# Kernel tuning notes

Hardware: AMD Instinct MI355X
Metric: run time of the kernel (lower is better)

## Reference

```python
import jax, jax.numpy as jnp
import numpy as np
from jax import lax

ANCHOR_SCALES = (64.0, 128.0, 256.0)
ANCHOR_RATIOS = (0.5, 1.0, 2.0)
STRIDE = 32
NMS_THRESH = 0.7


def make_anchors(feat_h, feat_w):
    base = []
    for s in ANCHOR_SCALES:
        for r in ANCHOR_RATIOS:
            w = s * np.sqrt(max(r, 1e-6))
            h = s / np.sqrt(max(r, 1e-6))
            base.append([-w / 2, -h / 2, w / 2, h / 2])
    base = jnp.asarray(base, jnp.float32)  # [A=9, 4]
    sx = jnp.arange(feat_w, dtype=jnp.float32) * STRIDE
    sy = jnp.arange(feat_h, dtype=jnp.float32) * STRIDE
    yy, xx = jnp.meshgrid(sy, sx, indexing='ij')
    shifts = jnp.stack([xx, yy, xx, yy], axis=2).reshape(-1, 4)  # [H*W, 4]
    # location-major, anchor-minor -> matches permute(0,2,3,1).view(B,-1,·)
    return (base[None, :, :] + shifts[:, None, :]).reshape(-1, 4)  # [N, 4]


def apply_deltas(anchors, deltas):
    w = anchors[:, 2] - anchors[:, 0]
    h = anchors[:, 3] - anchors[:, 1]
    cx = anchors[:, 0] + 0.5 * w
    cy = anchors[:, 1] + 0.5 * h
    pcx = deltas[:, 0] * w + cx
    pcy = deltas[:, 1] * h + cy
    pw = jnp.exp(deltas[:, 2]) * w
    ph = jnp.exp(deltas[:, 3]) * h
    return jnp.stack([pcx - 0.5 * pw, pcy - 0.5 * ph,
                      pcx + 0.5 * pw, pcy + 0.5 * ph], axis=1)


def pairwise_iou(b):
    area = (b[:, 2] - b[:, 0]) * (b[:, 3] - b[:, 1])
    lt = jnp.maximum(b[:, None, :2], b[None, :, :2])
    rb = jnp.minimum(b[:, None, 2:], b[None, :, 2:])
    wh = jnp.clip(rb - lt, 0.0)
    inter = wh[..., 0] * wh[..., 1]
    return inter / (area[:, None] + area[None, :] - inter)


def nms_keep(boxes, scores, thresh):
    # greedy NMS (torchvision semantics: suppress iou > thresh), returns bool keep mask
    n = boxes.shape[0]
    order = jnp.argsort(-scores)
    sb = boxes[order]
    idx = jnp.arange(n)
    sup_mat = (pairwise_iou(sb) > thresh) & (idx[None, :] > idx[:, None])

    def body(i, sup):
        return sup | ((~sup[i]) & sup_mat[i])

    sup = lax.fori_loop(0, n, body, jnp.zeros(n, bool))
    return jnp.zeros(n, bool).at[order].set(~sup)


def setup_inputs() -> dict:
    key = jax.random.key(0)
    ks = jax.random.split(key, 4)
    features = jax.random.normal(ks[0], (4, 512, 25, 25), jnp.float32)
    conv_w = jax.random.normal(ks[1], (512, 512, 3, 3), jnp.float32) * 0.01
    conv_b = jnp.zeros((512,), jnp.float32)
    cls_w = jax.random.normal(ks[2], (18, 512), jnp.float32) * 0.01
    cls_b = jnp.zeros((18,), jnp.float32)
    bbox_w = jax.random.normal(ks[3], (36, 512), jnp.float32) * 0.01
    bbox_b = jnp.zeros((36,), jnp.float32)
    return {"features": features, "conv_w": conv_w, "conv_b": conv_b,
            "cls_w": cls_w, "cls_b": cls_b, "bbox_w": bbox_w, "bbox_b": bbox_b,
            "img_h": 800, "img_w": 800}


def reference(features, conv_w, conv_b, cls_w, cls_b, bbox_w, bbox_b, img_h, img_w):
    B, _, H, W = features.shape
    x = lax.conv_general_dilated(features, conv_w, (1, 1), 'SAME',
                                 dimension_numbers=('NCHW', 'OIHW', 'NCHW'))
    x = jax.nn.relu(x + conv_b[None, :, None, None])
    obj = jnp.einsum('bchw,oc->bohw', x, cls_w) + cls_b[None, :, None, None]
    dlt = jnp.einsum('bchw,oc->bohw', x, bbox_w) + bbox_b[None, :, None, None]
    obj = obj.transpose(0, 2, 3, 1).reshape(B, -1, 2)      # [B, N, 2]
    dlt = dlt.transpose(0, 2, 3, 1).reshape(B, -1, 4)      # [B, N, 4]

    anchors = make_anchors(H, W)                            # [N, 4]
    props = jax.vmap(lambda d: apply_deltas(anchors, d))(dlt)
    hi = jnp.asarray([img_w, img_h, img_w, img_h], jnp.float32)
    props = jnp.clip(props, 0.0, hi)                        # clip to image
    scores = jax.nn.softmax(obj, axis=-1)[..., 1]           # [B, N]
    keep = jax.vmap(lambda b, s: nms_keep(b, s, NMS_THRESH))(props, scores)
    # suppressed boxes zeroed (fixed-shape analogue of props[keep])
    return props * keep[..., None].astype(props.dtype)
```

## Files before the change

### kernel.cpp

```cpp
#include <hip/hip_runtime.h>


#define NBATCH 4
#define HWDIM  25
#define NPOS   625
#define NM     2500
#define CIN    512
#define NANCH  5625
#define NW     88
#define CAP    4096
#define SORTN  6144

typedef unsigned long long u64;
typedef unsigned int u32;

struct BaseAnchors { float x1[9], y1[9], x2[9], y2[9]; };

__device__ __forceinline__ u64 bcast64(u64 v, int lane) {
  unsigned int lo = (unsigned int)v;
  unsigned int hi = (unsigned int)(v >> 32);
  lo = (unsigned int)__builtin_amdgcn_readlane((int)lo, lane);
  hi = (unsigned int)__builtin_amdgcn_readlane((int)hi, lane);
  return (((u64)hi) << 32) | (u64)lo;
}

__device__ __forceinline__ u64 waveOr64(u64 x) {
  unsigned int lo = (unsigned int)x, hi = (unsigned int)(x >> 32);
#pragma unroll
  for (int off = 32; off > 0; off >>= 1) {
    lo |= (unsigned int)__shfl_xor((int)lo, off, 64);
    hi |= (unsigned int)__shfl_xor((int)hi, off, 64);
  }
  return (((u64)hi) << 32) | (u64)lo;
}


__global__ void transpose_features(const float* __restrict__ f, float* __restrict__ fm) {
  __shared__ float tile[32][33];
  int b  = blockIdx.z;
  int p0 = blockIdx.x * 32;
  int c0 = blockIdx.y * 32;
  int tx = threadIdx.x, ty = threadIdx.y;
#pragma unroll
  for (int j = 0; j < 4; j++) {
    int c = c0 + ty + j * 8;
    int p = p0 + tx;
    if (p < NPOS) tile[ty + j * 8][tx] = f[((size_t)(b * CIN + c)) * NPOS + p];
  }
  __syncthreads();
#pragma unroll
  for (int j = 0; j < 4; j++) {
    int p = p0 + ty + j * 8;
    int c = c0 + tx;
    if (p < NPOS) fm[((size_t)(b * NPOS + p)) * CIN + c] = tile[tx][ty + j * 8];
  }
}

__global__ __launch_bounds__(256) void transpose_weights(const float* __restrict__ cw,
                                                         float* __restrict__ Wt) {
  __shared__ float tile[32][289];
  int o0 = blockIdx.x * 32, c0 = blockIdx.y * 32;
  int tid = threadIdx.x;
#pragma unroll
  for (int j = 0; j < 36; j++) {
    int idx = tid + j * 256;
    int o = idx / 288, kk = idx % 288;
    tile[o][kk] = cw[((size_t)(o0 + o)) * 4608 + c0 * 9 + kk];
  }
  __syncthreads();
  int ol = tid & 31, pg = tid >> 5;
#pragma unroll
  for (int j = 0; j < 36; j++) {
    int pair = pg + j * 8;
    int c = pair / 9, tap = pair % 9;
    Wt[((size_t)tap * CIN + (c0 + c)) * 512 + o0 + ol] = tile[ol][pair];
  }
}

__global__ void build_wco(const float* __restrict__ clsw, const float* __restrict__ clsb,
                          const float* __restrict__ bw, const float* __restrict__ bbb,
                          float* __restrict__ Wco, float* __restrict__ bco) {
  int idx = blockIdx.x * 256 + threadIdx.x;
  if (idx < 512 * 64) {
    int c = idx >> 6, o = idx & 63;
    float v = 0.f;
    if (o < 18) v = clsw[o * 512 + c];
    else if (o < 54) v = bw[(o - 18) * 512 + c];
    Wco[idx] = v;
  }
  if (idx < 64) {
    float v = 0.f;
    if (idx < 18) v = clsb[idx];
    else if (idx < 54) v = bbb[idx - 18];
    bco[idx] = v;
  }
}

__global__ void zero_cnt(u32* __restrict__ cnt) {
  int i = blockIdx.x * 64 + threadIdx.x;
  if (i < NBATCH * NW) cnt[i] = 0u;
}

__global__ __launch_bounds__(256) void conv_gemm(const float* __restrict__ fm,
                                                 const float* __restrict__ Wt,
                                                 float* __restrict__ xp) {
  __shared__ __align__(16) float At[32][68];
  __shared__ __align__(16) float Bt[32][64];
  int tid = threadIdx.x;
  int m0 = blockIdx.x << 6;
  int o0 = blockIdx.y << 6;
  int part = blockIdx.z;
  int ti = tid >> 4, tj = tid & 15;
  int si = tid >> 2, sq = tid & 3;
  int skk = tid >> 3, sr = tid & 7;
  float acc[4][4] = {{0.f}};

  int m = m0 + si;
  bool mv = m < NM;
  int mm = mv ? m : 0;
  int bb = mm / NPOS, rem = mm % NPOS;
  int hh = rem / HWDIM, ww = rem % HWDIM;
  int dy = part - 1;

  for (int tt = 0; tt < 3; tt++) {
    int tap = part * 3 + tt;
    int dx = tt - 1;
    int h2 = hh + dy, w2 = ww + dx;
    bool av = mv && ((unsigned)h2 < (unsigned)HWDIM) && ((unsigned)w2 < (unsigned)HWDIM);
    const float* arow = fm + (((size_t)(bb * NPOS + h2 * HWDIM + w2)) << 9);
    const float* bbase = Wt + (((size_t)tap) << 18) + o0;

    float4 a0 = make_float4(0.f, 0.f, 0.f, 0.f), a1 = a0;
    if (av) {
      a0 = *(const float4*)(arow + (sq << 2));
      a1 = *(const float4*)(arow + 16 + (sq << 2));
    }
    const float* bp0 = bbase + (((size_t)skk) << 9);
    float4 b0 = *(const float4*)(bp0 + (sr << 2));
    float4 b1 = *(const float4*)(bp0 + 32 + (sr << 2));

    for (int c0 = 0; c0 < CIN; c0 += 32) {
      __syncthreads();
      int kb = sq << 2;
      At[kb + 0][si] = a0.x; At[kb + 1][si] = a0.y; At[kb + 2][si] = a0.z; At[kb + 3][si] = a0.w;
      At[kb + 16][si] = a1.x; At[kb + 17][si] = a1.y; At[kb + 18][si] = a1.z; At[kb + 19][si] = a1.w;
      *(float4*)&Bt[skk][sr << 2] = b0;
      *(float4*)&Bt[skk][32 + (sr << 2)] = b1;
      float4 na0 = make_float4(0.f, 0.f, 0.f, 0.f), na1 = na0;
      float4 nb0 = na0, nb1 = na0;
      int c1 = c0 + 32;
      if (c1 < CIN) {
        if (av) {
          na0 = *(const float4*)(arow + c1 + (sq << 2));
          na1 = *(const float4*)(arow + c1 + 16 + (sq << 2));
        }
        const float* bp = bbase + (((size_t)(c1 + skk)) << 9);
        nb0 = *(const float4*)(bp + (sr << 2));
        nb1 = *(const float4*)(bp + 32 + (sr << 2));
      }
      __syncthreads();
#pragma unroll
      for (int kk = 0; kk < 32; kk++) {
        float4 avv = *(const float4*)&At[kk][ti << 2];
        float4 bvv = *(const float4*)&Bt[kk][tj << 2];
        float a_[4] = {avv.x, avv.y, avv.z, avv.w};
        float b_[4] = {bvv.x, bvv.y, bvv.z, bvv.w};
#pragma unroll
        for (int u = 0; u < 4; u++)
#pragma unroll
          for (int v = 0; v < 4; v++) acc[u][v] += a_[u] * b_[v];
      }
      a0 = na0; a1 = na1; b0 = nb0; b1 = nb1;
    }
  }
  float* outp = xp + (size_t)part * (NM * 512);
#pragma unroll
  for (int u = 0; u < 4; u++) {
    int mr = m0 + (ti << 2) + u;
    if (mr < NM) {
      float4 r = make_float4(acc[u][0], acc[u][1], acc[u][2], acc[u][3]);
      *(float4*)(outp + (((size_t)mr) << 9) + o0 + (tj << 2)) = r;
    }
  }
}

__global__ void combine_relu(const float* __restrict__ xp, const float* __restrict__ bias,
                             float* __restrict__ x2) {
  int i4 = blockIdx.x * 256 + threadIdx.x;
  if (i4 >= NM * 128) return;
  float4 p0 = *(const float4*)(xp + (size_t)i4 * 4);
  float4 p1 = *(const float4*)(xp + (size_t)(NM * 512) + (size_t)i4 * 4);
  float4 p2 = *(const float4*)(xp + (size_t)(2 * NM * 512) + (size_t)i4 * 4);
  float4 bb = *(const float4*)(bias + (i4 & 127) * 4);
  float4 r;
  r.x = fmaxf(p0.x + p1.x + p2.x + bb.x, 0.f);
  r.y = fmaxf(p0.y + p1.y + p2.y + bb.y, 0.f);
  r.z = fmaxf(p0.z + p1.z + p2.z + bb.z, 0.f);
  r.w = fmaxf(p0.w + p1.w + p2.w + bb.w, 0.f);
  *(float4*)(x2 + (size_t)i4 * 4) = r;
}

__global__ __launch_bounds__(256) void gemm1x1(const float* __restrict__ x2,
                                               const float* __restrict__ Wco,
                                               const float* __restrict__ bco,
                                               float* __restrict__ logits) {
  __shared__ __align__(16) float At[32][68];
  __shared__ __align__(16) float Bt[32][64];
  int tid = threadIdx.x;
  int m0 = blockIdx.x << 6;
  int ti = tid >> 4, tj = tid & 15;
  int si = tid >> 2, sq = tid & 3;
  int skk = tid >> 3, sr = tid & 7;
  float acc[4][4] = {{0.f}};
  int m = m0 + si;
  bool mv = m < NM;
  const float* arow = x2 + (((size_t)(mv ? m : 0)) << 9);
  for (int c0 = 0; c0 < CIN; c0 += 32) {
    __syncthreads();
    float4 a0 = make_float4(0.f, 0.f, 0.f, 0.f), a1 = a0;
    if (mv) {
      a0 = *(const float4*)(arow + c0 + (sq << 2));
      a1 = *(const float4*)(arow + c0 + 16 + (sq << 2));
    }
    int kb = sq << 2;
    At[kb + 0][si] = a0.x; At[kb + 1][si] = a0.y; At[kb + 2][si] = a0.z; At[kb + 3][si] = a0.w;
    At[kb + 16][si] = a1.x; At[kb + 17][si] = a1.y; At[kb + 18][si] = a1.z; At[kb + 19][si] = a1.w;
    const float* bp = Wco + (size_t)(c0 + skk) * 64;
    *(float4*)&Bt[skk][sr << 2] = *(const float4*)(bp + (sr << 2));
    *(float4*)&Bt[skk][32 + (sr << 2)] = *(const float4*)(bp + 32 + (sr << 2));
    __syncthreads();
#pragma unroll
    for (int kk = 0; kk < 32; kk++) {
      float4 avv = *(const float4*)&At[kk][ti << 2];
      float4 bvv = *(const float4*)&Bt[kk][tj << 2];
      float a_[4] = {avv.x, avv.y, avv.z, avv.w};
      float b_[4] = {bvv.x, bvv.y, bvv.z, bvv.w};
#pragma unroll
      for (int u = 0; u < 4; u++)
#pragma unroll
        for (int v = 0; v < 4; v++) acc[u][v] += a_[u] * b_[v];
    }
  }
  float4 bias = *(const float4*)(bco + (tj << 2));
#pragma unroll
  for (int u = 0; u < 4; u++) {
    int mr = m0 + (ti << 2) + u;
    if (mr < NM) {
      float4 r = make_float4(acc[u][0] + bias.x, acc[u][1] + bias.y, acc[u][2] + bias.z,
                             acc[u][3] + bias.w);
      *(float4*)(logits + (size_t)mr * 64 + (tj << 2)) = r;
    }
  }
}

__global__ __launch_bounds__(256) void score_box_kernel(const float* __restrict__ logits,
                                                        const int* __restrict__ ih,
                                                        const int* __restrict__ iw,
                                                        BaseAnchors ba,
                                                        float* __restrict__ scores,
                                                        float* __restrict__ props) {
#pragma clang fp contract(off)
  int n = blockIdx.x * 256 + threadIdx.x;
  if (n >= NBATCH * NANCH) return;
  int b = n / NANCH;
  int r = n % NANCH;
  int pos = r / 9, aa = r % 9;
  int py = pos / HWDIM, px = pos % HWDIM;
  const float* L = logits + (size_t)(b * NPOS + pos) * 64;
  float l0 = L[2 * aa], l1 = L[2 * aa + 1];
  float mx = fmaxf(l0, l1);
  float e0 = expf(l0 - mx), e1 = expf(l1 - mx);
  float s = e1 / (e0 + e1);
  float d0 = L[18 + 4 * aa + 0], d1 = L[18 + 4 * aa + 1];
  float d2 = L[18 + 4 * aa + 2], d3 = L[18 + 4 * aa + 3];
  float xf = (float)px * 32.f, yf = (float)py * 32.f;
  float ax1 = ba.x1[aa] + xf, ay1 = ba.y1[aa] + yf;
  float ax2 = ba.x2[aa] + xf, ay2 = ba.y2[aa] + yf;
  float wA = ax2 - ax1, hA = ay2 - ay1;
  float cx = ax1 + 0.5f * wA, cy = ay1 + 0.5f * hA;
  float pcx = d0 * wA + cx, pcy = d1 * hA + cy;
  float pw = expf(d2) * wA, ph = expf(d3) * hA;
  float x1 = pcx - 0.5f * pw, y1 = pcy - 0.5f * ph;
  float x2 = pcx + 0.5f * pw, y2 = pcy + 0.5f * ph;
  float W = (float)iw[0], H = (float)ih[0];
  x1 = fminf(fmaxf(x1, 0.f), W);
  y1 = fminf(fmaxf(y1, 0.f), H);
  x2 = fminf(fmaxf(x2, 0.f), W);
  y2 = fminf(fmaxf(y2, 0.f), H);
  scores[n] = s;
  *(float4*)(props + (size_t)n * 4) = make_float4(x1, y1, x2, y2);
}

__global__ __launch_bounds__(1024, 1) void radix_sort_kernel(const float* __restrict__ scores,
                                                             const float* __restrict__ props,
                                                             int* __restrict__ order,
                                                             float* __restrict__ sb) {
  __shared__ u32 kA[SORTN], vA[SORTN], kB[SORTN], vB[SORTN];
  __shared__ u32 hist[16][256];
  __shared__ u32 tot[256], base[256], tmp[256];
  int b = blockIdx.x, tid = threadIdx.x;
  int lane = tid & 63, wv = tid >> 6;
  const float* sc = scores + (size_t)b * NANCH;

  for (int i = tid; i < SORTN; i += 1024) {
    kA[i] = (i < NANCH) ? __float_as_uint(sc[i]) : 0u;
    vA[i] = (u32)i;
  }
  __syncthreads();

  for (int pass = 0; pass < 4; pass++) {
    int shift = pass << 3;
    u32* ks = (pass & 1) ? kB : kA;
    u32* vs = (pass & 1) ? vB : vA;
    u32* kd = (pass & 1) ? kA : kB;
    u32* vd = (pass & 1) ? vA : vB;
    for (int i = tid; i < 4096; i += 1024) ((u32*)hist)[i] = 0u;
    __syncthreads();
    for (int r = 0; r < 6; r++) {
      int i = wv * 384 + (r << 6) + lane;
      u32 d = 255u - ((ks[i] >> shift) & 255u);
      atomicAdd(&hist[wv][d], 1u);
    }
    __syncthreads();
    if (tid < 256) {
      u32 run = 0;
#pragma unroll
      for (int w = 0; w < 16; w++) { u32 t = hist[w][tid]; hist[w][tid] = run; run += t; }
      tot[tid] = run;
    }
    __syncthreads();
    if (tid < 256) tmp[tid] = tot[tid];
    __syncthreads();
    for (int off = 1; off < 256; off <<= 1) {
      u32 v = 0;
      if (tid < 256 && tid >= off) v = tmp[tid - off];
      __syncthreads();
      if (tid < 256) tmp[tid] += v;
      __syncthreads();
    }
    if (tid < 256) base[tid] = tmp[tid] - tot[tid];
    __syncthreads();
    if (tid < 256) {
      u32 bs = base[tid];
#pragma unroll
      for (int w = 0; w < 16; w++) hist[w][tid] += bs;
    }
    __syncthreads();
    for (int r = 0; r < 6; r++) {
      int i = wv * 384 + (r << 6) + lane;
      u32 key = ks[i], val = vs[i];
      u32 d = 255u - ((key >> shift) & 255u);
      u64 grp = ~0ull;
#pragma unroll
      for (int bit = 0; bit < 8; bit++) {
        u64 bal = __ballot(((d >> bit) & 1u) != 0u);
        grp &= ((d >> bit) & 1u) ? bal : ~bal;
      }
      u64 ltmask = (1ull << lane) - 1ull;
      u32 rank = (u32)__popcll(grp & ltmask);
      int leader = (int)__builtin_ctzll(grp);
      u32 oldv = 0;
      if (lane == leader) oldv = atomicAdd(&hist[wv][d], (u32)__popcll(grp));
      oldv = (u32)__shfl((int)oldv, leader, 64);
      u32 slot = oldv + rank;
      kd[slot] = key;
      vd[slot] = val;
    }
    __syncthreads();
  }

  const float* pr = props + (size_t)b * NANCH * 4;
  for (int i = tid; i < NANCH; i += 1024) {
    u32 orig = vA[i];
    order[b * NANCH + i] = (int)orig;
    float4 p = *(const float4*)(pr + (size_t)orig * 4);
    *(float4*)(sb + ((size_t)b * NANCH + i) * 4) = p;
  }
}

__global__ __launch_bounds__(64) void nms_mask_kernel(const float* __restrict__ sb,
                                                      uint4* __restrict__ lists,
                                                      u32* __restrict__ cnt,
                                                      u64* __restrict__ maskd) {
#pragma clang fp contract(off)
  int rb = blockIdx.x, cb = blockIdx.y, b = blockIdx.z;
  if (cb < rb) return;
  int lane = threadIdx.x;
  __shared__ float4 cbox[64];
  int j0 = cb << 6;
  const float* sbb = sb + (size_t)b * NANCH * 4;
  if (j0 + lane < NANCH) cbox[lane] = *(const float4*)(sbb + (size_t)(j0 + lane) * 4);
  __syncthreads();
  int i = (rb << 6) + lane;
  if (i >= NANCH) return;
  float4 rbox = *(const float4*)(sbb + (size_t)i * 4);
  float rarea = (rbox.z - rbox.x) * (rbox.w - rbox.y);
  u64 bits = 0ull;
  int jmax = NANCH - j0;
  if (jmax > 64) jmax = 64;
  for (int l = 0; l < jmax; l++) {
    int j = j0 + l;
    if (j > i) {
      float4 c = cbox[l];
      float carea = (c.z - c.x) * (c.w - c.y);
      float ltx = fmaxf(rbox.x, c.x), lty = fmaxf(rbox.y, c.y);
      float rbx = fminf(rbox.z, c.z), rby = fminf(rbox.w, c.w);
      float wx = fmaxf(rbx - ltx, 0.f);
      float wy = fmaxf(rby - lty, 0.f);
      float inter = wx * wy;
      float iou = inter / (rarea + carea - inter);
      if (iou > 0.7f) bits |= (1ull << l);
    }
  }
  if (rb == cb) {
    maskd[((size_t)b * NW + rb) * 64 + lane] = bits;
  } else if (bits) {
    u32 idx = atomicAdd(&cnt[b * NW + cb], 1u);
    if (idx < CAP)
      lists[((size_t)(b * NW + cb)) * CAP + idx] =
          make_uint4((u32)bits, (u32)(bits >> 32), (u32)i, 0u);
  }
}

__global__ __launch_bounds__(64, 1) void nms_scan_kernel(const uint4* __restrict__ lists,
                                                         const u32* __restrict__ cnt,
                                                         const u64* __restrict__ maskd,
                                                         const int* __restrict__ order,
                                                         const float* __restrict__ sb,
                                                         float* __restrict__ out) {
  int b = blockIdx.x;
  int lane = threadIdx.x;
  __shared__ u64 keep_sh[NW];
  const u64* md = maskd + (size_t)b * NW * 64;
  const uint4* lb = lists + (size_t)b * NW * CAP;

  u32 c0 = (lane < NW) ? cnt[b * NW + lane] : 0u;
  u32 c1 = (lane + 64 < NW) ? cnt[b * NW + lane + 64] : 0u;

  u64 diag = md[lane];
  uint4 pf = lb[lane];
  for (int s = 0; s < NW; s++) {
    u64 Mw = diag;
    uint4 e0 = pf;
    if (s + 1 < NW) {
      diag = md[((s + 1) << 6) + lane];
      pf = lb[(size_t)(s + 1) * CAP + lane];
    }

    int cn = (int)(u32)__builtin_amdgcn_readlane(
        (int)((s < 64) ? c0 : c1), (s < 64) ? s : s - 64);
    if (cn > CAP) cn = CAP;

    u64 acc = 0ull;
    if (lane < cn) {
      u64 kw = keep_sh[e0.z >> 6];
      if ((kw >> (e0.z & 63)) & 1ull) acc |= (((u64)e0.y) << 32) | (u64)e0.x;
    }
    for (int p = lane + 64; p < cn; p += 64) {
      uint4 e = lb[(size_t)s * CAP + p];
      u64 kw = keep_sh[e.z >> 6];
      if ((kw >> (e.z & 63)) & 1ull) acc |= (((u64)e.y) << 32) | (u64)e.x;
    }
    u64 cur = waveOr64(acc);

    int nrows = NANCH - (s << 6);
    if (nrows > 64) nrows = 64;
    u64 valid = (nrows < 64) ? ((1ull << nrows) - 1ull) : ~0ull;

    u64 nz = __ballot(Mw != 0ull);
    u64 todo = nz & ~cur & valid;
    while (todo) {
      int t = (int)__builtin_ctzll(todo);
      cur |= bcast64(Mw, t);
      todo &= ~cur;
      todo &= ~(1ull << t);
    }
    u64 alive = (~cur) & valid;
    if (lane == 0) keep_sh[s] = alive;
  }

  for (int i = lane; i < NANCH; i += 64) {
    u64 kw = keep_sh[i >> 6];
    bool kept = ((kw >> (i & 63)) & 1ull) != 0ull;
    int orig = order[b * NANCH + i];
    float4 p = *(const float4*)(sb + ((size_t)b * NANCH + i) * 4);
    float4 o = kept ? p : make_float4(0.f, 0.f, 0.f, 0.f);
    *(float4*)(out + ((size_t)b * NANCH + orig) * 4) = o;
  }
}


extern "C" void kernel_launch(void* const* d_in, const int* in_sizes, int n_in,
                              void* d_out, int out_size, void* d_ws, size_t ws_size,
                              hipStream_t stream) {
  const float* features = (const float*)d_in[0];
  const float* conv_w   = (const float*)d_in[1];
  const float* conv_b   = (const float*)d_in[2];
  const float* cls_w    = (const float*)d_in[3];
  const float* cls_b    = (const float*)d_in[4];
  const float* bbox_w   = (const float*)d_in[5];
  const float* bbox_b   = (const float*)d_in[6];
  const int*   img_h    = (const int*)d_in[7];
  const int*   img_w    = (const int*)d_in[8];
  float* out = (float*)d_out;
  char* ws = (char*)d_ws;

  const size_t OFF_FM    = 0;
  const size_t OFF_WT    = 5120000;
  const size_t OFF_XP    = 14557184;
  const size_t OFF_LISTS = 0;
  const size_t OFF_CNT   = 23068672;
  const size_t OFF_MASKD = 23070208;
  const size_t OFF_X2  = 29917184;
  const size_t OFF_WCO = 35037184;
  const size_t OFF_BCO = 35168256;
  const size_t OFF_LOG = 35168512;
  const size_t OFF_SC  = 35808512;
  const size_t OFF_PR  = 35898512;
  const size_t OFF_ORD = 36258512;
  const size_t OFF_SB  = 36348512;
  const size_t WS_NEEDED = 36708512;
  if (ws_size < WS_NEEDED) return;

  float* fm   = (float*)(ws + OFF_FM);
  float* Wt   = (float*)(ws + OFF_WT);
  float* xp   = (float*)(ws + OFF_XP);
  uint4* lists = (uint4*)(ws + OFF_LISTS);
  u32*   cnt   = (u32*)(ws + OFF_CNT);
  u64*   maskd = (u64*)(ws + OFF_MASKD);
  float* x2   = (float*)(ws + OFF_X2);
  float* Wco  = (float*)(ws + OFF_WCO);
  float* bco  = (float*)(ws + OFF_BCO);
  float* logits = (float*)(ws + OFF_LOG);
  float* scores = (float*)(ws + OFF_SC);
  float* props  = (float*)(ws + OFF_PR);
  int*   order  = (int*)(ws + OFF_ORD);
  float* sb     = (float*)(ws + OFF_SB);

  BaseAnchors ba;
  {
    const double scales[3] = {64.0, 128.0, 256.0};
    const double ratios[3] = {0.5, 1.0, 2.0};
    int a = 0;
    for (int si = 0; si < 3; si++)
      for (int ri = 0; ri < 3; ri++, a++) {
        double w = scales[si] * sqrt(ratios[ri]);
        double h = scales[si] / sqrt(ratios[ri]);
        ba.x1[a] = (float)(-w / 2.0);
        ba.y1[a] = (float)(-h / 2.0);
        ba.x2[a] = (float)(w / 2.0);
        ba.y2[a] = (float)(h / 2.0);
      }
  }

  transpose_features<<<dim3(20, 16, 4), dim3(32, 8), 0, stream>>>(features, fm);
  transpose_weights<<<dim3(16, 16), 256, 0, stream>>>(conv_w, Wt);
  build_wco<<<128, 256, 0, stream>>>(cls_w, cls_b, bbox_w, bbox_b, Wco, bco);
  conv_gemm<<<dim3(40, 8, 3), 256, 0, stream>>>(fm, Wt, xp);
  combine_relu<<<1250, 256, 0, stream>>>(xp, conv_b, x2);
  gemm1x1<<<40, 256, 0, stream>>>(x2, Wco, bco, logits);
  score_box_kernel<<<88, 256, 0, stream>>>(logits, img_h, img_w, ba, scores, props);
  radix_sort_kernel<<<4, 1024, 0, stream>>>(scores, props, order, sb);
  zero_cnt<<<6, 64, 0, stream>>>(cnt);
  nms_mask_kernel<<<dim3(NW, NW, 4), 64, 0, stream>>>(sb, lists, cnt, maskd);
  nms_scan_kernel<<<4, 64, 0, stream>>>(lists, cnt, maskd, order, sb, out);
}
```

Baseline: 390.0 us.

## Fuse prep kernels and fold split-K combine and scoring into head GEMM

Merges the feature transpose, weight transpose, head-weight packing and counter zeroing into one block-indexed prep kernel. Folds the split-K partial sum, bias and ReLU into the A-tile load of the 1x1 head GEMM, and computes softmax scores and decoded boxes from a shared-memory logits tile in the same kernel. This removes several launches and the x2 and logits round trips through global memory. In exchange, the head GEMM with only 40 blocks now reads three partial buffers directly, and the workspace offsets for the counters and mask are moved.

```diff
diff --git a/kernel.cpp b/kernel.cpp
--- a/kernel.cpp
+++ b/kernel.cpp
@@ -34,71 +34,67 @@
   return (((u64)hi) << 32) | (u64)lo;
 }
 
-
-__global__ void transpose_features(const float* __restrict__ f, float* __restrict__ fm) {
-  __shared__ float tile[32][33];
-  int b  = blockIdx.z;
-  int p0 = blockIdx.x * 32;
-  int c0 = blockIdx.y * 32;
-  int tx = threadIdx.x, ty = threadIdx.y;
-#pragma unroll
-  for (int j = 0; j < 4; j++) {
-    int c = c0 + ty + j * 8;
-    int p = p0 + tx;
-    if (p < NPOS) tile[ty + j * 8][tx] = f[((size_t)(b * CIN + c)) * NPOS + p];
-  }
-  __syncthreads();
-#pragma unroll
-  for (int j = 0; j < 4; j++) {
-    int p = p0 + ty + j * 8;
-    int c = c0 + tx;
-    if (p < NPOS) fm[((size_t)(b * NPOS + p)) * CIN + c] = tile[tx][ty + j * 8];
-  }
-}
-
-__global__ __launch_bounds__(256) void transpose_weights(const float* __restrict__ cw,
-                                                         float* __restrict__ Wt) {
-  __shared__ float tile[32][289];
-  int o0 = blockIdx.x * 32, c0 = blockIdx.y * 32;
+__global__ __launch_bounds__(256) void prep_kernel(
+    const float* __restrict__ f, float* __restrict__ fm,
+    const float* __restrict__ cw, float* __restrict__ Wt,
+    const float* __restrict__ clsw, const float* __restrict__ clsb,
+    const float* __restrict__ bw, const float* __restrict__ bbb,
+    float* __restrict__ Wco, float* __restrict__ bco, u32* __restrict__ cnt) {
+  __shared__ float shbuf[32 * 289];
+  int B = blockIdx.x;
   int tid = threadIdx.x;
-#pragma unroll
-  for (int j = 0; j < 36; j++) {
-    int idx = tid + j * 256;
-    int o = idx / 288, kk = idx % 288;
-    tile[o][kk] = cw[((size_t)(o0 + o)) * 4608 + c0 * 9 + kk];
-  }
-  __syncthreads();
-  int ol = tid & 31, pg = tid >> 5;
-#pragma unroll
-  for (int j = 0; j < 36; j++) {
-    int pair = pg + j * 8;
-    int c = pair / 9, tap = pair % 9;
-    Wt[((size_t)tap * CIN + (c0 + c)) * 512 + o0 + ol] = tile[ol][pair];
-  }
-}
-
-__global__ void build_wco(const float* __restrict__ clsw, const float* __restrict__ clsb,
-                          const float* __restrict__ bw, const float* __restrict__ bbb,
-                          float* __restrict__ Wco, float* __restrict__ bco) {
-  int idx = blockIdx.x * 256 + threadIdx.x;
-  if (idx < 512 * 64) {
-    int c = idx >> 6, o = idx & 63;
-    float v = 0.f;
-    if (o < 18) v = clsw[o * 512 + c];
-    else if (o < 54) v = bw[(o - 18) * 512 + c];
-    Wco[idx] = v;
-  }
-  if (idx < 64) {
-    float v = 0.f;
-    if (idx < 18) v = clsb[idx];
-    else if (idx < 54) v = bbb[idx - 18];
-    bco[idx] = v;
-  }
-}
-
-__global__ void zero_cnt(u32* __restrict__ cnt) {
-  int i = blockIdx.x * 64 + threadIdx.x;
-  if (i < NBATCH * NW) cnt[i] = 0u;
+  if (B < 1280) {
+    int bx = B % 20, by = (B / 20) % 16, b = B / 320;
+    int p0 = bx * 32, c0 = by * 32;
+    int tx = tid & 31, ty = tid >> 5;
+#pragma unroll
+    for (int j = 0; j < 4; j++) {
+      int c = c0 + ty + j * 8;
+      int p = p0 + tx;
+      if (p < NPOS) shbuf[(ty + j * 8) * 33 + tx] = f[((size_t)(b * CIN + c)) * NPOS + p];
+    }
+    __syncthreads();
+#pragma unroll
+    for (int j = 0; j < 4; j++) {
+      int p = p0 + ty + j * 8;
+      int c = c0 + tx;
+      if (p < NPOS) fm[((size_t)(b * NPOS + p)) * CIN + c] = shbuf[tx * 33 + ty + j * 8];
+    }
+  } else if (B < 1536) {
+    int idx0 = B - 1280;
+    int o0 = (idx0 & 15) * 32, c0 = (idx0 >> 4) * 32;
+#pragma unroll
+    for (int j = 0; j < 36; j++) {
+      int idx = tid + j * 256;
+      int o = idx / 288, kk = idx % 288;
+      shbuf[o * 289 + kk] = cw[((size_t)(o0 + o)) * 4608 + c0 * 9 + kk];
+    }
+    __syncthreads();
+    int ol = tid & 31, pg = tid >> 5;
+#pragma unroll
+    for (int j = 0; j < 36; j++) {
+      int pair = pg + j * 8;
+      int c = pair / 9, tap = pair % 9;
+      Wt[((size_t)tap * CIN + (c0 + c)) * 512 + o0 + ol] = shbuf[ol * 289 + pair];
+    }
+  } else if (B < 1664) {
+    int idx = (B - 1536) * 256 + tid;
+    if (idx < 512 * 64) {
+      int c = idx >> 6, o = idx & 63;
+      float v = 0.f;
+      if (o < 18) v = clsw[o * 512 + c];
+      else if (o < 54) v = bw[(o - 18) * 512 + c];
+      Wco[idx] = v;
+    }
+    if (B == 1536 && idx < 64) {
+      float v = 0.f;
+      if (idx < 18) v = clsb[idx];
+      else if (idx < 54) v = bbb[idx - 18];
+      bco[idx] = v;
+    }
+  } else {
+    for (int i = tid; i < NBATCH * NW; i += 256) cnt[i] = 0u;
+  }
 }
 
 __global__ __launch_bounds__(256) void conv_gemm(const float* __restrict__ fm,
@@ -184,28 +180,18 @@
   }
 }
 
-__global__ void combine_relu(const float* __restrict__ xp, const float* __restrict__ bias,
-                             float* __restrict__ x2) {
-  int i4 = blockIdx.x * 256 + threadIdx.x;
-  if (i4 >= NM * 128) return;
-  float4 p0 = *(const float4*)(xp + (size_t)i4 * 4);
-  float4 p1 = *(const float4*)(xp + (size_t)(NM * 512) + (size_t)i4 * 4);
-  float4 p2 = *(const float4*)(xp + (size_t)(2 * NM * 512) + (size_t)i4 * 4);
-  float4 bb = *(const float4*)(bias + (i4 & 127) * 4);
-  float4 r;
-  r.x = fmaxf(p0.x + p1.x + p2.x + bb.x, 0.f);
-  r.y = fmaxf(p0.y + p1.y + p2.y + bb.y, 0.f);
-  r.z = fmaxf(p0.z + p1.z + p2.z + bb.z, 0.f);
-  r.w = fmaxf(p0.w + p1.w + p2.w + bb.w, 0.f);
-  *(float4*)(x2 + (size_t)i4 * 4) = r;
-}
-
-__global__ __launch_bounds__(256) void gemm1x1(const float* __restrict__ x2,
-                                               const float* __restrict__ Wco,
-                                               const float* __restrict__ bco,
-                                               float* __restrict__ logits) {
+__global__ __launch_bounds__(256) void head_kernel(const float* __restrict__ xp,
+                                                   const float* __restrict__ convb,
+                                                   const float* __restrict__ Wco,
+                                                   const float* __restrict__ bco,
+                                                   const int* __restrict__ ih,
+                                                   const int* __restrict__ iw,
+                                                   BaseAnchors ba,
+                                                   float* __restrict__ scores,
+                                                   float* __restrict__ props) {
   __shared__ __align__(16) float At[32][68];
   __shared__ __align__(16) float Bt[32][64];
+  __shared__ float Lt[64][65];
   int tid = threadIdx.x;
   int m0 = blockIdx.x << 6;
   int ti = tid >> 4, tj = tid & 15;
@@ -214,13 +200,29 @@
   float acc[4][4] = {{0.f}};
   int m = m0 + si;
   bool mv = m < NM;
-  const float* arow = x2 + (((size_t)(mv ? m : 0)) << 9);
+  const float* base = xp + (((size_t)(mv ? m : 0)) << 9);
   for (int c0 = 0; c0 < CIN; c0 += 32) {
     __syncthreads();
     float4 a0 = make_float4(0.f, 0.f, 0.f, 0.f), a1 = a0;
     if (mv) {
-      a0 = *(const float4*)(arow + c0 + (sq << 2));
-      a1 = *(const float4*)(arow + c0 + 16 + (sq << 2));
+      int e0 = c0 + (sq << 2);
+      float4 p0 = *(const float4*)(base + e0);
+      float4 p1 = *(const float4*)(base + (size_t)(NM * 512) + e0);
+      float4 p2 = *(const float4*)(base + (size_t)(2 * NM * 512) + e0);
+      float4 bb = *(const float4*)(convb + e0);
+      a0.x = fmaxf(p0.x + p1.x + p2.x + bb.x, 0.f);
+      a0.y = fmaxf(p0.y + p1.y + p2.y + bb.y, 0.f);
+      a0.z = fmaxf(p0.z + p1.z + p2.z + bb.z, 0.f);
+      a0.w = fmaxf(p0.w + p1.w + p2.w + bb.w, 0.f);
+      int e1 = e0 + 16;
+      float4 q0 = *(const float4*)(base + e1);
+      float4 q1 = *(const float4*)(base + (size_t)(NM * 512) + e1);
+      float4 q2 = *(const float4*)(base + (size_t)(2 * NM * 512) + e1);
+      float4 cb = *(const float4*)(convb + e1);
+      a1.x = fmaxf(q0.x + q1.x + q2.x + cb.x, 0.f);
+      a1.y = fmaxf(q0.y + q1.y + q2.y + cb.y, 0.f);
+      a1.z = fmaxf(q0.z + q1.z + q2.z + cb.z, 0.f);
+      a1.w = fmaxf(q0.w + q1.w + q2.w + cb.w, 0.f);
     }
     int kb = sq << 2;
     At[kb + 0][si] = a0.x; At[kb + 1][si] = a0.y; At[kb + 2][si] = a0.z; At[kb + 3][si] = a0.w;
@@ -244,51 +246,46 @@
   float4 bias = *(const float4*)(bco + (tj << 2));
 #pragma unroll
   for (int u = 0; u < 4; u++) {
-    int mr = m0 + (ti << 2) + u;
-    if (mr < NM) {
-      float4 r = make_float4(acc[u][0] + bias.x, acc[u][1] + bias.y, acc[u][2] + bias.z,
-                             acc[u][3] + bias.w);
-      *(float4*)(logits + (size_t)mr * 64 + (tj << 2)) = r;
-    }
-  }
-}
-
-__global__ __launch_bounds__(256) void score_box_kernel(const float* __restrict__ logits,
-                                                        const int* __restrict__ ih,
-                                                        const int* __restrict__ iw,
-                                                        BaseAnchors ba,
-                                                        float* __restrict__ scores,
-                                                        float* __restrict__ props) {
+    int row = (ti << 2) + u;
+    Lt[row][(tj << 2) + 0] = acc[u][0] + bias.x;
+    Lt[row][(tj << 2) + 1] = acc[u][1] + bias.y;
+    Lt[row][(tj << 2) + 2] = acc[u][2] + bias.z;
+    Lt[row][(tj << 2) + 3] = acc[u][3] + bias.w;
+  }
+  __syncthreads();
+  {
 #pragma clang fp contract(off)
-  int n = blockIdx.x * 256 + threadIdx.x;
-  if (n >= NBATCH * NANCH) return;
-  int b = n / NANCH;
-  int r = n % NANCH;
-  int pos = r / 9, aa = r % 9;
-  int py = pos / HWDIM, px = pos % HWDIM;
-  const float* L = logits + (size_t)(b * NPOS + pos) * 64;
-  float l0 = L[2 * aa], l1 = L[2 * aa + 1];
-  float mx = fmaxf(l0, l1);
-  float e0 = expf(l0 - mx), e1 = expf(l1 - mx);
-  float s = e1 / (e0 + e1);
-  float d0 = L[18 + 4 * aa + 0], d1 = L[18 + 4 * aa + 1];
-  float d2 = L[18 + 4 * aa + 2], d3 = L[18 + 4 * aa + 3];
-  float xf = (float)px * 32.f, yf = (float)py * 32.f;
-  float ax1 = ba.x1[aa] + xf, ay1 = ba.y1[aa] + yf;
-  float ax2 = ba.x2[aa] + xf, ay2 = ba.y2[aa] + yf;
-  float wA = ax2 - ax1, hA = ay2 - ay1;
-  float cx = ax1 + 0.5f * wA, cy = ay1 + 0.5f * hA;
-  float pcx = d0 * wA + cx, pcy = d1 * hA + cy;
-  float pw = expf(d2) * wA, ph = expf(d3) * hA;
-  float x1 = pcx - 0.5f * pw, y1 = pcy - 0.5f * ph;
-  float x2 = pcx + 0.5f * pw, y2 = pcy + 0.5f * ph;
-  float W = (float)iw[0], H = (float)ih[0];
-  x1 = fminf(fmaxf(x1, 0.f), W);
-  y1 = fminf(fmaxf(y1, 0.f), H);
-  x2 = fminf(fmaxf(x2, 0.f), W);
-  y2 = fminf(fmaxf(y2, 0.f), H);
-  scores[n] = s;
-  *(float4*)(props + (size_t)n * 4) = make_float4(x1, y1, x2, y2);
+    for (int it = tid; it < 576; it += 256) {
+      int mrel = it / 9, aa = it % 9;
+      int mm2 = m0 + mrel;
+      if (mm2 >= NM) continue;
+      int b = mm2 / NPOS, pos = mm2 % NPOS;
+      int py = pos / HWDIM, px = pos % HWDIM;
+      float l0 = Lt[mrel][2 * aa], l1 = Lt[mrel][2 * aa + 1];
+      float mx = fmaxf(l0, l1);
+      float e0 = expf(l0 - mx), e1 = expf(l1 - mx);
+      float s = e1 / (e0 + e1);
+      float d0 = Lt[mrel][18 + 4 * aa + 0], d1 = Lt[mrel][18 + 4 * aa + 1];
+      float d2 = Lt[mrel][18 + 4 * aa + 2], d3 = Lt[mrel][18 + 4 * aa + 3];
+      float xf = (float)px * 32.f, yf = (float)py * 32.f;
+      float ax1 = ba.x1[aa] + xf, ay1 = ba.y1[aa] + yf;
+      float ax2 = ba.x2[aa] + xf, ay2 = ba.y2[aa] + yf;
+      float wA = ax2 - ax1, hA = ay2 - ay1;
+      float cx = ax1 + 0.5f * wA, cy = ay1 + 0.5f * hA;
+      float pcx = d0 * wA + cx, pcy = d1 * hA + cy;
+      float pw = expf(d2) * wA, ph = expf(d3) * hA;
+      float x1 = pcx - 0.5f * pw, y1 = pcy - 0.5f * ph;
+      float x2 = pcx + 0.5f * pw, y2 = pcy + 0.5f * ph;
+      float W = (float)iw[0], H = (float)ih[0];
+      x1 = fminf(fmaxf(x1, 0.f), W);
+      y1 = fminf(fmaxf(y1, 0.f), H);
+      x2 = fminf(fmaxf(x2, 0.f), W);
+      y2 = fminf(fmaxf(y2, 0.f), H);
+      int n = b * NANCH + pos * 9 + aa;
+      scores[n] = s;
+      *(float4*)(props + (size_t)n * 4) = make_float4(x1, y1, x2, y2);
+    }
+  }
 }
 
 __global__ __launch_bounds__(1024, 1) void radix_sort_kernel(const float* __restrict__ scores,
@@ -509,12 +506,10 @@
   const size_t OFF_WT    = 5120000;
   const size_t OFF_XP    = 14557184;
   const size_t OFF_LISTS = 0;
-  const size_t OFF_CNT   = 23068672;
-  const size_t OFF_MASKD = 23070208;
-  const size_t OFF_X2  = 29917184;
+  const size_t OFF_CNT   = 29917184;
+  const size_t OFF_MASKD = 29919232;
   const size_t OFF_WCO = 35037184;
   const size_t OFF_BCO = 35168256;
-  const size_t OFF_LOG = 35168512;
   const size_t OFF_SC  = 35808512;
   const size_t OFF_PR  = 35898512;
   const size_t OFF_ORD = 36258512;
@@ -528,10 +523,8 @@
   uint4* lists = (uint4*)(ws + OFF_LISTS);
   u32*   cnt   = (u32*)(ws + OFF_CNT);
   u64*   maskd = (u64*)(ws + OFF_MASKD);
-  float* x2   = (float*)(ws + OFF_X2);
   float* Wco  = (float*)(ws + OFF_WCO);
   float* bco  = (float*)(ws + OFF_BCO);
-  float* logits = (float*)(ws + OFF_LOG);
   float* scores = (float*)(ws + OFF_SC);
   float* props  = (float*)(ws + OFF_PR);
   int*   order  = (int*)(ws + OFF_ORD);
@@ -553,15 +546,12 @@
       }
   }
 
-  transpose_features<<<dim3(20, 16, 4), dim3(32, 8), 0, stream>>>(features, fm);
-  transpose_weights<<<dim3(16, 16), 256, 0, stream>>>(conv_w, Wt);
-  build_wco<<<128, 256, 0, stream>>>(cls_w, cls_b, bbox_w, bbox_b, Wco, bco);
+  prep_kernel<<<1665, 256, 0, stream>>>(features, fm, conv_w, Wt,
+                                        cls_w, cls_b, bbox_w, bbox_b, Wco, bco, cnt);
   conv_gemm<<<dim3(40, 8, 3), 256, 0, stream>>>(fm, Wt, xp);
-  combine_relu<<<1250, 256, 0, stream>>>(xp, conv_b, x2);
-  gemm1x1<<<40, 256, 0, stream>>>(x2, Wco, bco, logits);
-  score_box_kernel<<<88, 256, 0, stream>>>(logits, img_h, img_w, ba, scores, props);
+  head_kernel<<<40, 256, 0, stream>>>(xp, conv_b, Wco, bco, img_h, img_w, ba,
+                                      scores, props);
   radix_sort_kernel<<<4, 1024, 0, stream>>>(scores, props, order, sb);
-  zero_cnt<<<6, 64, 0, stream>>>(cnt);
   nms_mask_kernel<<<dim3(NW, NW, 4), 64, 0, stream>>>(sb, lists, cnt, maskd);
   nms_scan_kernel<<<4, 64, 0, stream>>>(lists, cnt, maskd, order, sb, out);
 }
```

Measured after the change: 391.4 us (median of 2 runs). Within noise of the previous version (+0.4%).
